# Performance work log

Measured on AMD Instinct MI355X. Metric: run time of the kernel, lower is better.

Reference implementation:

```python
import jax, jax.numpy as jnp
import numpy as np

UNITS = 50257
CUTOFF = [2000, 10000, UNITS]   # cutoff + [units], as in __init__
D = 1024
FACTOR = 4
N_CLUST = len(CUTOFF) - 1       # 2 tail clusters
HEAD_OUT = CUTOFF[0] + N_CLUST  # 2002 = head classes + one logit per cluster


def _tail_dims():
    dims = []
    for i in range(N_CLUST):
        dim = D / FACTOR ** (i + 1)
        dims.append(max(1, round(dim / 8)) * 8)
    return dims  # [256, 64]


def setup_inputs() -> dict:
    key = jax.random.key(0)
    ks = jax.random.split(key, 16)
    B, T = 2, 1024
    x = jax.random.normal(ks[0], (B, T, D), jnp.float32)
    targets = jax.random.randint(ks[1], (B, T), 0, UNITS)
    inp = {
        'x': x,
        'targets': targets,
        # head: Dense(D -> HEAD_OUT), use_bias=False (glorot-ish scaling)
        'head_kernel': jax.random.normal(ks[2], (D, HEAD_OUT), jnp.float32) / np.float32(np.sqrt(D)),
    }
    for i, dim in enumerate(_tail_dims()):
        out = CUTOFF[i + 1] - CUTOFF[i]
        inp[f'proj_kernel_{i}'] = jax.random.normal(ks[3 + 4 * i], (D, dim), jnp.float32) / np.float32(np.sqrt(D))
        inp[f'proj_bias_{i}'] = jnp.zeros((dim,), jnp.float32)
        inp[f'scale_kernel_{i}'] = jax.random.normal(ks[4 + 4 * i], (dim, out), jnp.float32) / np.float32(np.sqrt(dim))
        inp[f'scale_bias_{i}'] = jnp.zeros((out,), jnp.float32)
    return inp


def reference(x, targets, head_kernel,
              proj_kernel_0, proj_bias_0, scale_kernel_0, scale_bias_0,
              proj_kernel_1, proj_bias_1, scale_kernel_1, scale_bias_1):
    # Head: root logits over [head classes | cluster logits]
    root_logits = jnp.einsum('btd,dh->bth', x, head_kernel)          # [B,T,HEAD_OUT]
    root_logprobs = jax.nn.log_softmax(root_logits, axis=-1)
    parts = [root_logprobs[..., :CUTOFF[0]]]                          # head class logprobs
    tails = [(proj_kernel_0, proj_bias_0, scale_kernel_0, scale_bias_0),
             (proj_kernel_1, proj_bias_1, scale_kernel_1, scale_bias_1)]
    for i, (pk, pb, sk, sb) in enumerate(tails):
        h = jnp.einsum('btd,dk->btk', x, pk) + pb                     # low-rank projection
        logits = jnp.einsum('btk,kv->btv', h, sk) + sb                # cluster vocab slice
        clust_lp = root_logprobs[..., CUTOFF[0] + i:CUTOFF[0] + i + 1]
        parts.append(jax.nn.log_softmax(logits, axis=-1) + clust_lp)  # P(w) = P(cluster)*P(w|cluster)
    logprobs = jnp.concatenate(parts, axis=-1)                        # [B,T,UNITS]
    return jnp.exp(logprobs)
```

## Files before the change

### kernel.cpp

```cpp
#include <hip/hip_runtime.h>
#include <cstdint>
#include <cstddef>

#define ROWS    2048
#define DIM     1024
#define VOCAB   50257
#define CUT0    2000
#define CUT1    10000
#define PROJ_LD 320
#define LGTC_LD 10016

typedef __attribute__((ext_vector_type(8))) _Float16 f16x8;
typedef __attribute__((ext_vector_type(4))) float    f32x4;
typedef __attribute__((ext_vector_type(4))) unsigned int u32x4;

__device__ __forceinline__ void gload_lds16(const void* g, void* l) {
    __builtin_amdgcn_global_load_lds(
        (const __attribute__((address_space(1))) void*)g,
        (__attribute__((address_space(3))) void*)l, 16, 0, 0);
}

__device__ __forceinline__ int swz8(int i, int n) {
    return (i & 7) * (n >> 3) + (i >> 3);
}

__device__ __forceinline__ void transpose_tile(
    const float* __restrict__ src, _Float16* __restrict__ dst,
    int K, int N, int local, int ntiles, float* tile)
{
    const int t  = threadIdx.x;
    const int bn = local % ntiles, bk = local / ntiles;
    const int tx = t & 31, ty = t >> 5;
    const int n0 = bn * 32, k0 = bk * 32;
#pragma unroll
    for (int i = 0; i < 4; ++i) {
        int kk = ty + i * 8;
        int n  = n0 + tx;
        tile[kk * 33 + tx] = (n < N) ? src[(size_t)(k0 + kk) * N + n] : 0.f;
    }
    __syncthreads();
#pragma unroll
    for (int i = 0; i < 4; ++i) {
        int nn = ty + i * 8;
        int r  = n0 + nn;
        dst[(size_t)r * K + k0 + tx] = (_Float16)tile[tx * 33 + nn];
    }
}

__global__ __launch_bounds__(256)
void convert_all(const float* __restrict__ x, const float* __restrict__ head,
                 const float* __restrict__ pk0, const float* __restrict__ pk1,
                 const float* __restrict__ sk0, const float* __restrict__ sk1,
                 _Float16* __restrict__ A, _Float16* __restrict__ headT,
                 _Float16* __restrict__ pkT, _Float16* __restrict__ sk0T,
                 _Float16* __restrict__ sk1T, float* __restrict__ S)
{
    __shared__ float tile[32 * 33];
    const int bid = blockIdx.x, t = threadIdx.x;

    if (bid >= 9016) {
        int i = (bid - 9016) * 256 + t;
        ((float4*)S)[i] = make_float4(0.f, 0.f, 0.f, 0.f);
        return;
    }
    if (bid < 2048) {
        int fid = bid * 256 + t;
        float4 v = ((const float4*)x)[fid];
        union { _Float16 h[4]; ushort4 u; } cv;
        cv.h[0] = (_Float16)v.x; cv.h[1] = (_Float16)v.y;
        cv.h[2] = (_Float16)v.z; cv.h[3] = (_Float16)v.w;
        ((ushort4*)A)[fid] = cv.u;
        return;
    }
    if (bid < 4096)
        transpose_tile(head, headT, 1024, 2002, bid - 2048, 64, tile);
    else if (bid < 4352)
        transpose_tile(pk0, pkT, 1024, 256, bid - 4096, 8, tile);
    else if (bid < 4480)
        transpose_tile(pk1, pkT + 256 * 1024, 1024, 64, bid - 4352, 4, tile);
    else if (bid < 6496)
        transpose_tile(sk0, sk0T, 256, 8000, bid - 4480, 252, tile);
    else
        transpose_tile(sk1, sk1T, 64, 40257, bid - 6496, 1260, tile);
}

template<int MODE, int BM>
__device__ __forceinline__ void gemm_dbuf(
    _Float16* As, _Float16* Bs,
    const _Float16* __restrict__ A, int lda,
    const _Float16* __restrict__ B, int K,
    int bx, int by, int Nvalid,
    const float* __restrict__ pb0, const float* __restrict__ pb1,
    _Float16* __restrict__ lgtC, float* __restrict__ root2,
    float* __restrict__ S, _Float16* __restrict__ h)
{
    const int t    = threadIdx.x;
    const int lane = t & 63;
    const int w    = t >> 6;
    const int wr   = w >> 1, wc = w & 1;
    const int q    = lane >> 4, cl = lane & 15;
    const int row0blk = by * BM;
    const int col0blk = bx * 128;
    constexpr int MR   = BM / 32;
    constexpr int NISS = MR + 4;

    float bn4p[4] = {0.f, 0.f, 0.f, 0.f};
    if (MODE == 3) {
#pragma unroll
        for (int n = 0; n < 4; ++n) {
            int colseg = col0blk + wc * 64 + n * 16 + cl;
            if (colseg < PROJ_LD)
                bn4p[n] = (colseg < 256) ? pb0[colseg] : pb1[colseg - 256];
        }
    }
    __builtin_amdgcn_sched_barrier(0);

    f32x4 acc[MR][4];
#pragma unroll
    for (int m = 0; m < MR; ++m)
#pragma unroll
        for (int n = 0; n < 4; ++n)
            acc[m][n] = (f32x4){0.f, 0.f, 0.f, 0.f};

    auto stage = [&](int bufi, int k0) {
        _Float16* Asb = As + bufi * (BM * 64);
        _Float16* Bsb = Bs + bufi * (128 * 64);
#pragma unroll
        for (int iss = 0; iss < MR; ++iss) {
            int ci  = iss * 256 + w * 64 + lane;
            int row = ci >> 3;
            int ch  = (ci & 7) ^ (row & 7);
            gload_lds16(A + (size_t)(row0blk + row) * lda + k0 + ch * 8,
                        Asb + (size_t)(iss * 256 + w * 64) * 8);
        }
#pragma unroll
        for (int iss = 0; iss < 4; ++iss) {
            int ci  = iss * 256 + w * 64 + lane;
            int row = ci >> 3;
            int ch  = (ci & 7) ^ (row & 7);
            gload_lds16(B + (size_t)(col0blk + row) * K + k0 + ch * 8,
                        Bsb + (size_t)(iss * 256 + w * 64) * 8);
        }
    };

    const int nsteps = K / 64;
    stage(0, 0);
    int cur = 0;
    for (int ts = 0; ts < nsteps; ++ts) {
        if (ts + 1 < nsteps) {
            stage(cur ^ 1, (ts + 1) * 64);
            asm volatile("s_waitcnt vmcnt(%0)" :: "n"(NISS) : "memory");
        } else {
            asm volatile("s_waitcnt vmcnt(0)" ::: "memory");
        }
        __builtin_amdgcn_s_barrier();
        __builtin_amdgcn_sched_barrier(0);

        const _Float16* Asb = As + cur * (BM * 64);
        const _Float16* Bsb = Bs + cur * (128 * 64);
#pragma unroll
        for (int kk = 0; kk < 2; ++kk) {
            f16x8 a[MR], b[4];
#pragma unroll
            for (int m = 0; m < MR; ++m) {
                int row = wr * (BM / 2) + m * 16 + cl;
                int ch  = (kk * 4 + q) ^ (row & 7);
                a[m] = *(const f16x8*)(Asb + row * 64 + ch * 8);
            }
#pragma unroll
            for (int n = 0; n < 4; ++n) {
                int row = wc * 64 + n * 16 + cl;
                int ch  = (kk * 4 + q) ^ (row & 7);
                b[n] = *(const f16x8*)(Bsb + row * 64 + ch * 8);
            }
#pragma unroll
            for (int m = 0; m < MR; ++m)
#pragma unroll
                for (int n = 0; n < 4; ++n)
                    acc[m][n] = __builtin_amdgcn_mfma_f32_16x16x32_f16(
                        a[m], b[n], acc[m][n], 0, 0, 0);
        }
        __builtin_amdgcn_sched_barrier(0);
        __builtin_amdgcn_s_barrier();
        cur ^= 1;
    }
    __syncthreads();

    if (MODE == 3) {
#pragma unroll
        for (int m = 0; m < MR; ++m)
#pragma unroll
            for (int n = 0; n < 4; ++n) {
                int colseg = col0blk + wc * 64 + n * 16 + cl;
                if (colseg < PROJ_LD) {
#pragma unroll
                    for (int j = 0; j < 4; ++j) {
                        int rg = row0blk + wr * (BM / 2) + m * 16 + q * 4 + j;
                        h[(size_t)rg * PROJ_LD + colseg] =
                            (_Float16)(acc[m][n][j] + bn4p[n]);
                    }
                }
            }
        return;
    }

    float* sred = (float*)As;
#pragma unroll
    for (int m = 0; m < MR; ++m)
#pragma unroll
        for (int j = 0; j < 4; ++j) {
            int rloc = wr * (BM / 2) + m * 16 + q * 4 + j;
            int rg   = row0blk + rloc;
            float sm = 0.f;
#pragma unroll
            for (int n = 0; n < 4; ++n) {
                int c = col0blk + wc * 64 + n * 16 + cl;
                float v = acc[m][n][j];
                bool ok = c < Nvalid;
                if (ok) {
                    if (c < CUT0)
                        lgtC[(size_t)rg * LGTC_LD + c] = (_Float16)v;
                    else
                        root2[rg * 2 + (c - CUT0)] = v;
                }
                sm += ok ? __expf(v) : 0.f;
            }
#pragma unroll
            for (int d = 1; d < 16; d <<= 1)
                sm += __shfl_xor(sm, d);
            if (cl == 0) sred[wc * BM + rloc] = sm;
        }
    __syncthreads();
    if (t < BM)
        atomicAdd(&S[(row0blk + t) * 4 + 0], sred[t] + sred[BM + t]);
}

template<int MODE, int BM>
__device__ __forceinline__ void gemm_body(
    _Float16* As, _Float16* Bs,
    const _Float16* __restrict__ A, int lda,
    const _Float16* __restrict__ B, int K,
    int bx, int by, int Nvalid,
    const float* __restrict__ bias,
    _Float16* __restrict__ lgtC, const float* __restrict__ root2,
    float* __restrict__ S, float* __restrict__ outF)
{
    const int t    = threadIdx.x;
    const int lane = t & 63;
    const int w    = t >> 6;
    const int wr   = w >> 1, wc = w & 1;
    const int q    = lane >> 4, cl = lane & 15;
    const int row0blk = by * BM;
    const int col0blk = bx * 128;
    constexpr int MR = BM / 32;

    f32x4 acc[MR][4];
#pragma unroll
    for (int m = 0; m < MR; ++m)
#pragma unroll
        for (int n = 0; n < 4; ++n)
            acc[m][n] = (f32x4){0.f, 0.f, 0.f, 0.f};

    for (int k0 = 0; k0 < K; k0 += 64) {
        __syncthreads();
#pragma unroll
        for (int iss = 0; iss < MR; ++iss) {
            int ci  = iss * 256 + w * 64 + lane;
            int row = ci >> 3;
            int ch  = (ci & 7) ^ (row & 7);
            gload_lds16(A + (size_t)(row0blk + row) * lda + k0 + ch * 8,
                        As + (size_t)(iss * 256 + w * 64) * 8);
        }
#pragma unroll
        for (int iss = 0; iss < 4; ++iss) {
            int ci  = iss * 256 + w * 64 + lane;
            int row = ci >> 3;
            int ch  = (ci & 7) ^ (row & 7);
            gload_lds16(B + (size_t)(col0blk + row) * K + k0 + ch * 8,
                        Bs + (size_t)(iss * 256 + w * 64) * 8);
        }
        __syncthreads();

#pragma unroll
        for (int kk = 0; kk < 2; ++kk) {
            f16x8 a[MR], b[4];
#pragma unroll
            for (int m = 0; m < MR; ++m) {
                int row = wr * (BM / 2) + m * 16 + cl;
                int ch  = (kk * 4 + q) ^ (row & 7);
                a[m] = *(const f16x8*)(As + row * 64 + ch * 8);
            }
#pragma unroll
            for (int n = 0; n < 4; ++n) {
                int row = wc * 64 + n * 16 + cl;
                int ch  = (kk * 4 + q) ^ (row & 7);
                b[n] = *(const f16x8*)(Bs + row * 64 + ch * 8);
            }
#pragma unroll
            for (int m = 0; m < MR; ++m)
#pragma unroll
                for (int n = 0; n < 4; ++n)
                    acc[m][n] = __builtin_amdgcn_mfma_f32_16x16x32_f16(
                        a[m], b[n], acc[m][n], 0, 0, 0);
        }
    }
    __syncthreads();

    float bn4[4];
#pragma unroll
    for (int n = 0; n < 4; ++n) {
        int colseg = col0blk + wc * 64 + n * 16 + cl;
        bn4[n] = (colseg < Nvalid) ? bias[colseg] : 0.f;
    }

    if (MODE == 4) {
#pragma unroll
        for (int m = 0; m < MR; ++m)
#pragma unroll
            for (int j = 0; j < 4; ++j) {
                int rg = row0blk + wr * (BM / 2) + m * 16 + q * 4 + j;
                float4 S4 = ((const float4*)S)[rg];
                float scl = __expf(root2[rg * 2 + 1]) / (S4.z * S4.x);
                size_t rb = (size_t)rg * VOCAB + CUT1;
#pragma unroll
                for (int n = 0; n < 4; ++n) {
                    int c = col0blk + wc * 64 + n * 16 + cl;
                    if (c < Nvalid)
                        outF[rb + c] = __expf(acc[m][n][j] + bn4[n]) * scl;
                }
            }
        return;
    }

    float* sred = (float*)As;
#pragma unroll
    for (int m = 0; m < MR; ++m)
#pragma unroll
        for (int j = 0; j < 4; ++j) {
            int rloc = wr * (BM / 2) + m * 16 + q * 4 + j;
            int rg   = row0blk + rloc;
            float sm = 0.f;
#pragma unroll
            for (int n = 0; n < 4; ++n) {
                int c = col0blk + wc * 64 + n * 16 + cl;
                float v = acc[m][n][j] + bn4[n];
                bool ok = c < Nvalid;
                if (MODE == 1 && ok)
                    lgtC[(size_t)rg * LGTC_LD + CUT0 + c] = (_Float16)v;
                sm += ok ? __expf(v) : 0.f;
            }
#pragma unroll
            for (int d = 1; d < 16; d <<= 1)
                sm += __shfl_xor(sm, d);
            if (cl == 0) sred[wc * BM + rloc] = sm;
        }
    __syncthreads();
    if (t < BM) {
        const int sidx = (MODE == 1) ? 1 : 2;
        atomicAdd(&S[(row0blk + t) * 4 + sidx], sred[t] + sred[BM + t]);
    }
}

__global__ __launch_bounds__(256)
void k2_projroot(const _Float16* __restrict__ A, const _Float16* __restrict__ pkT,
                 const _Float16* __restrict__ headT,
                 const float* __restrict__ pb0, const float* __restrict__ pb1,
                 _Float16* __restrict__ h, _Float16* __restrict__ lgtC,
                 float* __restrict__ root2, float* __restrict__ S)
{
    __shared__ _Float16 As[2 * 128 * 64];
    __shared__ _Float16 Bs[2 * 128 * 64];
    const int bid = blockIdx.x;
    if (bid < 512) {
        int i = swz8(bid, 512);
        gemm_dbuf<0, 64>(As, Bs, A, DIM, headT, 1024, i % 16, i / 16, 2002,
                         nullptr, nullptr, lgtC, root2, S, nullptr);
    } else {
        int i = swz8(bid - 512, 48);
        gemm_dbuf<3, 128>(As, Bs, A, DIM, pkT, 1024, i % 3, i / 3, PROJ_LD,
                          pb0, pb1, nullptr, nullptr, nullptr, h);
    }
}

__global__ __launch_bounds__(256)
void k3_scales(const _Float16* __restrict__ h, const _Float16* __restrict__ sk0T,
               const _Float16* __restrict__ sk1T,
               const float* __restrict__ sb0, const float* __restrict__ sb1,
               _Float16* __restrict__ lgtC, float* __restrict__ S)
{
    __shared__ _Float16 As[128 * 64];
    __shared__ _Float16 Bs[128 * 64];
    const int bid = blockIdx.x;
    if (bid < 1008) {
        int i = swz8(bid, 1008);
        gemm_body<1, 128>(As, Bs, h, PROJ_LD, sk0T, 256, i / 16, i % 16, 8000,
                          sb0, lgtC, nullptr, S, nullptr);
    } else {
        int i = swz8(bid - 1008, 5040);
        gemm_body<2, 128>(As, Bs, h + 256, PROJ_LD, sk1T, 64, i / 16, i % 16,
                          40257, sb1, nullptr, nullptr, S, nullptr);
    }
}

__global__ __launch_bounds__(256)
void k4_megafin(const _Float16* __restrict__ h, const _Float16* __restrict__ sk1T,
                const float* __restrict__ sb1, const _Float16* __restrict__ lgtC,
                const float* __restrict__ root2, const float* __restrict__ S,
                float* __restrict__ outF)
{
    __shared__ _Float16 As[128 * 64];
    __shared__ _Float16 Bs[128 * 64];
    const int bid = blockIdx.x;
    if (bid >= 2048) {
        int i = swz8(bid - 2048, 5040);
        gemm_body<4, 128>(As, Bs, h + 256, PROJ_LD, sk1T, 64, i / 16, i % 16,
                          40257, sb1, nullptr, root2, (float*)S, outF);
        return;
    }
    const int r = bid;
    float4 S4 = ((const float4*)S)[r];
    float inv_r = 1.f / S4.x;
    float sc0   = __expf(root2[r * 2 + 0]) / (S4.y * S4.x);
    const _Float16* lrow = lgtC + (size_t)r * LGTC_LD;
    float* orow = outF + (size_t)r * VOCAB;
    for (int i8 = threadIdx.x; i8 < CUT1 / 8; i8 += 256) {
        u32x4 raw = *(const u32x4*)(lrow + i8 * 8);
        union { uint32_t u; _Float16 hh[2]; } pp[4];
        pp[0].u = raw.x; pp[1].u = raw.y; pp[2].u = raw.z; pp[3].u = raw.w;
        const int c0 = i8 * 8;
        const float sc = (c0 < CUT0) ? inv_r : sc0;
        f32x4 o0, o1;
        o0.x = __expf((float)pp[0].hh[0]) * sc;
        o0.y = __expf((float)pp[0].hh[1]) * sc;
        o0.z = __expf((float)pp[1].hh[0]) * sc;
        o0.w = __expf((float)pp[1].hh[1]) * sc;
        o1.x = __expf((float)pp[2].hh[0]) * sc;
        o1.y = __expf((float)pp[2].hh[1]) * sc;
        o1.z = __expf((float)pp[3].hh[0]) * sc;
        o1.w = __expf((float)pp[3].hh[1]) * sc;
        *(f32x4*)(orow + c0)     = o0;
        *(f32x4*)(orow + c0 + 4) = o1;
    }
}

extern "C" void kernel_launch(void* const* d_in, const int* in_sizes, int n_in,
                              void* d_out, int out_size, void* d_ws, size_t ws_size,
                              hipStream_t stream)
{
    (void)in_sizes; (void)n_in; (void)out_size; (void)ws_size;

    const float* x    = (const float*)d_in[0];
    const float* head = (const float*)d_in[2];
    const float* pk0  = (const float*)d_in[3];
    const float* pb0  = (const float*)d_in[4];
    const float* sk0  = (const float*)d_in[5];
    const float* sb0  = (const float*)d_in[6];
    const float* pk1  = (const float*)d_in[7];
    const float* pb1  = (const float*)d_in[8];
    const float* sk1  = (const float*)d_in[9];
    const float* sb1  = (const float*)d_in[10];

    float* out = (float*)d_out;
    char*  ws  = (char*)d_ws;

    _Float16* lgtC  = (_Float16*)(ws);
    _Float16* A     = (_Float16*)(ws + 41025536);
    _Float16* headT = (_Float16*)(ws + 45219840);
    _Float16* pkT   = (_Float16*)(ws + 49414144);
    _Float16* sk0T  = (_Float16*)(ws + 50200576);
    _Float16* sk1T  = (_Float16*)(ws + 54329344);
    _Float16* h     = (_Float16*)(ws + 59490304);
    float*    root2 = (float*)(ws + 60801024);
    float*    S     = (float*)(ws + 60817408);

    const dim3 blk(256);

    convert_all<<<dim3(9024), blk, 0, stream>>>(x, head, pk0, pk1, sk0, sk1,
                                                A, headT, pkT, sk0T, sk1T, S);
    k2_projroot<<<dim3(560), blk, 0, stream>>>(A, pkT, headT, pb0, pb1,
                                               h, lgtC, root2, S);
    k3_scales<<<dim3(6048), blk, 0, stream>>>(h, sk0T, sk1T, sb0, sb1, lgtC, S);
    k4_megafin<<<dim3(7088), blk, 0, stream>>>(h, sk1T, sb1, lgtC, root2, S, out);
}
```

Before: 233.3 us.

## Replace per-tile cluster-1 GEMM with panel kernel reusing B tile across row tiles

The K=64 cluster-1 scale GEMM (used twice, once for sum-exp and once for the output write) now runs in a new panel routine. Each block loads one 128-column B tile into LDS once and loops over four 128-row A tiles with double-buffered async loads. This cuts the number of blocks and the redundant B reloads and per-block setup. The trade-off is fewer blocks for parallelism, more LDS per block (three tiles), and per-row atomics issued inside the loop in the sum pass.

```diff
diff --git a/kernel.cpp b/kernel.cpp
--- a/kernel.cpp
+++ b/kernel.cpp
@@ -313,25 +313,6 @@
         bn4[n] = (colseg < Nvalid) ? bias[colseg] : 0.f;
     }
 
-    if (MODE == 4) {
-#pragma unroll
-        for (int m = 0; m < MR; ++m)
-#pragma unroll
-            for (int j = 0; j < 4; ++j) {
-                int rg = row0blk + wr * (BM / 2) + m * 16 + q * 4 + j;
-                float4 S4 = ((const float4*)S)[rg];
-                float scl = __expf(root2[rg * 2 + 1]) / (S4.z * S4.x);
-                size_t rb = (size_t)rg * VOCAB + CUT1;
-#pragma unroll
-                for (int n = 0; n < 4; ++n) {
-                    int c = col0blk + wc * 64 + n * 16 + cl;
-                    if (c < Nvalid)
-                        outF[rb + c] = __expf(acc[m][n][j] + bn4[n]) * scl;
-                }
-            }
-        return;
-    }
-
     float* sred = (float*)As;
 #pragma unroll
     for (int m = 0; m < MR; ++m)
@@ -345,7 +326,7 @@
                 int c = col0blk + wc * 64 + n * 16 + cl;
                 float v = acc[m][n][j] + bn4[n];
                 bool ok = c < Nvalid;
-                if (MODE == 1 && ok)
+                if (ok)
                     lgtC[(size_t)rg * LGTC_LD + CUT0 + c] = (_Float16)v;
                 sm += ok ? __expf(v) : 0.f;
             }
@@ -355,9 +336,135 @@
             if (cl == 0) sred[wc * BM + rloc] = sm;
         }
     __syncthreads();
-    if (t < BM) {
-        const int sidx = (MODE == 1) ? 1 : 2;
-        atomicAdd(&S[(row0blk + t) * 4 + sidx], sred[t] + sred[BM + t]);
+    if (t < BM)
+        atomicAdd(&S[(row0blk + t) * 4 + 1], sred[t] + sred[BM + t]);
+}
+
+template<int MODE>
+__device__ __forceinline__ void gemm_panel(
+    _Float16* Bp, _Float16* Aab,
+    const _Float16* __restrict__ A,
+    const _Float16* __restrict__ B,
+    int bx, int g,
+    const float* __restrict__ bias,
+    const float* __restrict__ root2, float* __restrict__ S,
+    float* __restrict__ outF)
+{
+    const int t    = threadIdx.x;
+    const int lane = t & 63;
+    const int w    = t >> 6;
+    const int wr   = w >> 1, wc = w & 1;
+    const int q    = lane >> 4, cl = lane & 15;
+    const int col0 = bx * 128;
+    constexpr int T = 4;
+
+#pragma unroll
+    for (int iss = 0; iss < 4; ++iss) {
+        int ci  = iss * 256 + w * 64 + lane;
+        int row = ci >> 3;
+        int ch  = (ci & 7) ^ (row & 7);
+        gload_lds16(B + (size_t)(col0 + row) * 64 + ch * 8,
+                    Bp + (size_t)(iss * 256 + w * 64) * 8);
+    }
+    auto stageA = [&](int bufi, int ti) {
+        _Float16* Ab = Aab + bufi * (128 * 64);
+        int row0 = (g * T + ti) * 128;
+#pragma unroll
+        for (int iss = 0; iss < 4; ++iss) {
+            int ci  = iss * 256 + w * 64 + lane;
+            int row = ci >> 3;
+            int ch  = (ci & 7) ^ (row & 7);
+            gload_lds16(A + (size_t)(row0 + row) * PROJ_LD + ch * 8,
+                        Ab + (size_t)(iss * 256 + w * 64) * 8);
+        }
+    };
+    stageA(0, 0);
+
+    float bn4[4];
+#pragma unroll
+    for (int n = 0; n < 4; ++n) {
+        int c = col0 + wc * 64 + n * 16 + cl;
+        bn4[n] = (c < VOCAB - CUT1) ? bias[c] : 0.f;
+    }
+    __builtin_amdgcn_sched_barrier(0);
+
+    int cur = 0;
+    for (int ti = 0; ti < T; ++ti) {
+        asm volatile("s_waitcnt vmcnt(0)" ::: "memory");
+        __builtin_amdgcn_s_barrier();
+        __builtin_amdgcn_sched_barrier(0);
+        if (ti + 1 < T) stageA(cur ^ 1, ti + 1);
+
+        f32x4 acc[4][4];
+#pragma unroll
+        for (int m = 0; m < 4; ++m)
+#pragma unroll
+            for (int n = 0; n < 4; ++n)
+                acc[m][n] = (f32x4){0.f, 0.f, 0.f, 0.f};
+
+        const _Float16* Ab = Aab + cur * (128 * 64);
+#pragma unroll
+        for (int kk = 0; kk < 2; ++kk) {
+            f16x8 a[4], b[4];
+#pragma unroll
+            for (int m = 0; m < 4; ++m) {
+                int row = wr * 64 + m * 16 + cl;
+                int ch  = (kk * 4 + q) ^ (row & 7);
+                a[m] = *(const f16x8*)(Ab + row * 64 + ch * 8);
+            }
+#pragma unroll
+            for (int n = 0; n < 4; ++n) {
+                int row = wc * 64 + n * 16 + cl;
+                int ch  = (kk * 4 + q) ^ (row & 7);
+                b[n] = *(const f16x8*)(Bp + row * 64 + ch * 8);
+            }
+#pragma unroll
+            for (int m = 0; m < 4; ++m)
+#pragma unroll
+                for (int n = 0; n < 4; ++n)
+                    acc[m][n] = __builtin_amdgcn_mfma_f32_16x16x32_f16(
+                        a[m], b[n], acc[m][n], 0, 0, 0);
+        }
+
+        const int row0 = (g * T + ti) * 128;
+        if (MODE == 2) {
+#pragma unroll
+            for (int m = 0; m < 4; ++m)
+#pragma unroll
+                for (int j = 0; j < 4; ++j) {
+                    int rg = row0 + wr * 64 + m * 16 + q * 4 + j;
+                    float sm = 0.f;
+#pragma unroll
+                    for (int n = 0; n < 4; ++n) {
+                        int c = col0 + wc * 64 + n * 16 + cl;
+                        float v = acc[m][n][j] + bn4[n];
+                        sm += (c < VOCAB - CUT1) ? __expf(v) : 0.f;
+                    }
+#pragma unroll
+                    for (int d = 1; d < 16; d <<= 1)
+                        sm += __shfl_xor(sm, d);
+                    if (cl == 0) atomicAdd(&S[rg * 4 + 2], sm);
+                }
+        } else {
+#pragma unroll
+            for (int m = 0; m < 4; ++m)
+#pragma unroll
+                for (int j = 0; j < 4; ++j) {
+                    int rg = row0 + wr * 64 + m * 16 + q * 4 + j;
+                    float4 S4 = ((const float4*)S)[rg];
+                    float scl = __expf(root2[rg * 2 + 1]) / (S4.z * S4.x);
+                    size_t rb = (size_t)rg * VOCAB + CUT1;
+#pragma unroll
+                    for (int n = 0; n < 4; ++n) {
+                        int c = col0 + wc * 64 + n * 16 + cl;
+                        if (c < VOCAB - CUT1)
+                            outF[rb + c] = __expf(acc[m][n][j] + bn4[n]) * scl;
+                    }
+                }
+        }
+        __builtin_amdgcn_sched_barrier(0);
+        __builtin_amdgcn_s_barrier();
+        cur ^= 1;
     }
 }
 
@@ -388,17 +495,16 @@
                const float* __restrict__ sb0, const float* __restrict__ sb1,
                _Float16* __restrict__ lgtC, float* __restrict__ S)
 {
-    __shared__ _Float16 As[128 * 64];
-    __shared__ _Float16 Bs[128 * 64];
+    __shared__ _Float16 lds[3 * 128 * 64];
     const int bid = blockIdx.x;
     if (bid < 1008) {
         int i = swz8(bid, 1008);
-        gemm_body<1, 128>(As, Bs, h, PROJ_LD, sk0T, 256, i / 16, i % 16, 8000,
-                          sb0, lgtC, nullptr, S, nullptr);
+        gemm_body<1, 128>(lds, lds + 128 * 64, h, PROJ_LD, sk0T, 256,
+                          i / 16, i % 16, 8000, sb0, lgtC, nullptr, S, nullptr);
     } else {
-        int i = swz8(bid - 1008, 5040);
-        gemm_body<2, 128>(As, Bs, h + 256, PROJ_LD, sk1T, 64, i / 16, i % 16,
-                          40257, sb1, nullptr, nullptr, S, nullptr);
+        int i = bid - 1008;
+        gemm_panel<2>(lds, lds + 128 * 64, h + 256, sk1T, i / 4, i % 4,
+                      sb1, nullptr, S, nullptr);
     }
 }
 
@@ -408,13 +514,12 @@
                 const float* __restrict__ root2, const float* __restrict__ S,
                 float* __restrict__ outF)
 {
-    __shared__ _Float16 As[128 * 64];
-    __shared__ _Float16 Bs[128 * 64];
+    __shared__ _Float16 lds[3 * 128 * 64];
     const int bid = blockIdx.x;
     if (bid >= 2048) {
-        int i = swz8(bid - 2048, 5040);
-        gemm_body<4, 128>(As, Bs, h + 256, PROJ_LD, sk1T, 64, i / 16, i % 16,
-                          40257, sb1, nullptr, root2, (float*)S, outF);
+        int i = bid - 2048;
+        gemm_panel<4>(lds, lds + 128 * 64, h + 256, sk1T, i / 4, i % 4,
+                      sb1, root2, (float*)S, outF);
         return;
     }
     const int r = bid;
@@ -479,6 +584,6 @@
                                                 A, headT, pkT, sk0T, sk1T, S);
     k2_projroot<<<dim3(560), blk, 0, stream>>>(A, pkT, headT, pb0, pb1,
                                                h, lgtC, root2, S);
-    k3_scales<<<dim3(6048), blk, 0, stream>>>(h, sk0T, sk1T, sb0, sb1, lgtC, S);
-    k4_megafin<<<dim3(7088), blk, 0, stream>>>(h, sk1T, sb1, lgtC, root2, S, out);
-}
+    k3_scales<<<dim3(2268), blk, 0, stream>>>(h, sk0T, sk1T, sb0, sb1, lgtC, S);
+    k4_megafin<<<dim3(3308), blk, 0, stream>>>(h, sk1T, sb1, lgtC, root2, S, out);
+}
```

Result: slower. 316.4 us (+35.6%).
